# Kernel tuning notes

Measured on AMD Instinct MI355X. Metric: run time of the kernel, lower is better.

The kernel has to match this reference:

```python
import jax, jax.numpy as jnp
import numpy as np

PI = 3.141592653  # same constant as the torch source
M = 4
MIN_LAMBDA = 5.0
MAX_LAMBDA = 1500.0
IT = 1  # first forward call


def setup_inputs() -> dict:
    key = jax.random.key(0)
    k1, k2, k3 = jax.random.split(key, 3)
    N, D, C = 512, 512, 100000
    x = jax.random.normal(k1, (N, D), dtype=jnp.float32)
    target = jax.random.randint(k2, (N,), 0, C, dtype=jnp.int64)
    weight = jax.random.normal(k3, (D, C), dtype=jnp.float32)
    return {"x": x, "target": target, "weight": weight}


def reference(x, target, weight):
    # normalize weight columns (dim=0), as in F.normalize(w, p=2, dim=0)
    w = weight / jnp.linalg.norm(weight, axis=0, keepdims=True)
    w_norm = jnp.linalg.norm(w, axis=0, keepdims=True)          # [1, C] (~1)
    x_norm = jnp.linalg.norm(x, axis=1, keepdims=True)          # [N, 1]

    cos_theta = x @ w                                           # [N, C]
    cos_theta = jnp.clip(cos_theta / x_norm / w_norm, -1.0, 1.0)

    rows = jnp.arange(x.shape[0])
    c_t = cos_theta[rows, target]                               # [N]
    # m=4 multi-angle: cos(4t) = 8c^4 - 8c^2 + 1
    cos_m_theta = 8.0 * c_t ** 4 - 8.0 * c_t ** 2 + 1.0
    theta = jnp.arccos(c_t)
    k = jnp.floor(M * theta / PI)
    sign = 1.0 - 2.0 * (k % 2.0)                                # (-1)^k for integer-valued float k
    phi_t = sign * cos_m_theta - 2.0 * k

    cur_lambda = max(MIN_LAMBDA, MAX_LAMBDA / (1.0 + 0.1 * IT))
    addition = (phi_t - c_t) * x_norm[:, 0] / (1.0 + cur_lambda)

    out = cos_theta * x_norm                                    # [N, C]
    out = out.at[rows, target].add(addition)
    return out
```

## Files before the change

kernel.cpp:

```cpp
#include <hip/hip_runtime.h>
#include <hip/hip_bf16.h>

typedef __attribute__((ext_vector_type(4))) float f32x4;
typedef __attribute__((ext_vector_type(8))) short s16x8;

#define NR 512
#define KD 512
#define CC 100000
#define BN 32
#define LDSK 40

static __device__ __forceinline__ unsigned short f2bf(float f) {
    union { float f; unsigned u; } v; v.f = f;
    unsigned r = v.u + 0x7FFFu + ((v.u >> 16) & 1u);
    return (unsigned short)(r >> 16);
}

__global__ __launch_bounds__(256) void prep_kernel(const float* __restrict__ x,
                                                   float* __restrict__ xn,
                                                   unsigned short* __restrict__ xb) {
    const int row = blockIdx.x;
    const int t = threadIdx.x;
    const float* xr = x + row * KD;
    float v0 = xr[t];
    float v1 = xr[t + 256];
    float ss = v0 * v0 + v1 * v1;
    #pragma unroll
    for (int off = 32; off > 0; off >>= 1) ss += __shfl_down(ss, off, 64);
    __shared__ float sred[4];
    if ((t & 63) == 0) sred[t >> 6] = ss;
    __syncthreads();
    if (t == 0) xn[row] = sqrtf(sred[0] + sred[1] + sred[2] + sred[3]);
    xb[row * KD + t]       = f2bf(v0);
    xb[row * KD + t + 256] = f2bf(v1);
}

__global__ __launch_bounds__(256, 3) void gemm_kernel(const float* __restrict__ w,
                                                      const unsigned short* __restrict__ xb,
                                                      const float* __restrict__ xn,
                                                      float* __restrict__ out) {
    __shared__ unsigned short ldsB[BN * LDSK];
    __shared__ float sPart[8][BN];
    __shared__ float sInv[BN];

    const int t    = threadIdx.x;
    const int lane = t & 63;
    const int wv   = t >> 6;
    const int c0   = blockIdx.x * BN;
    const int cL   = t & 31;
    const int kq   = t >> 5;

    f32x4 acc[8][2];
    #pragma unroll
    for (int i = 0; i < 8; ++i) {
        acc[i][0] = {0.f, 0.f, 0.f, 0.f};
        acc[i][1] = {0.f, 0.f, 0.f, 0.f};
    }

    float ss = 0.0f;
    const int rowbase = wv * 128;
    const int arow = lane & 15;
    const int akq  = lane >> 4;

    const float* wp0 = w + (size_t)(kq * 4) * CC + c0 + cL;
    float bc0 = wp0[0];
    float bc1 = wp0[(size_t)CC];
    float bc2 = wp0[(size_t)2 * CC];
    float bc3 = wp0[(size_t)3 * CC];

    const unsigned short* abase = xb + (rowbase + arow) * KD + akq * 8;

    #pragma unroll 1
    for (int it = 0; it < 16; ++it) {
        const int kk = it * 32;

        s16x8 af[8];
        #pragma unroll
        for (int rt = 0; rt < 8; ++rt)
            af[rt] = *(const s16x8*)(abase + rt * 16 * KD + kk);

        float bn0 = 0.f, bn1 = 0.f, bn2 = 0.f, bn3 = 0.f;
        if (it < 15) {
            const float* wp = w + (size_t)(kk + 32 + kq * 4) * CC + c0 + cL;
            bn0 = wp[0];
            bn1 = wp[(size_t)CC];
            bn2 = wp[(size_t)2 * CC];
            bn3 = wp[(size_t)3 * CC];
        }

        ss += bc0 * bc0 + bc1 * bc1 + bc2 * bc2 + bc3 * bc3;
        ushort4 pk;
        pk.x = f2bf(bc0);
        pk.y = f2bf(bc1);
        pk.z = f2bf(bc2);
        pk.w = f2bf(bc3);

        __syncthreads();
        *(ushort4*)&ldsB[cL * LDSK + kq * 4] = pk;
        __syncthreads();

        const s16x8 bf0 = *(const s16x8*)&ldsB[(0 * 16 + arow) * LDSK + akq * 8];
        const s16x8 bf1 = *(const s16x8*)&ldsB[(1 * 16 + arow) * LDSK + akq * 8];

        #pragma unroll
        for (int rt = 0; rt < 8; ++rt) {
            acc[rt][0] = __builtin_amdgcn_mfma_f32_16x16x32_bf16(af[rt], bf0, acc[rt][0], 0, 0, 0);
            acc[rt][1] = __builtin_amdgcn_mfma_f32_16x16x32_bf16(af[rt], bf1, acc[rt][1], 0, 0, 0);
        }
        bc0 = bn0; bc1 = bn1; bc2 = bn2; bc3 = bn3;
    }

    sPart[kq][cL] = ss;
    __syncthreads();
    if (t < BN) {
        float tot = 0.f;
        #pragma unroll
        for (int i = 0; i < 8; ++i) tot += sPart[i][t];
        sInv[t] = 1.0f / sqrtf(tot);
    }
    __syncthreads();

    #pragma unroll
    for (int rt = 0; rt < 8; ++rt) {
        const int rbase = rowbase + rt * 16 + akq * 4;
        const f32x4 xnv = *(const f32x4*)(xn + rbase);
        #pragma unroll
        for (int ct = 0; ct < 2; ++ct) {
            const float inv = sInv[ct * 16 + arow];
            float* op = out + (size_t)rbase * CC + c0 + ct * 16 + arow;
            #pragma unroll
            for (int r = 0; r < 4; ++r) {
                float cv = acc[rt][ct][r] * inv / xnv[r];
                cv = fminf(1.0f, fmaxf(-1.0f, cv));
                op[(size_t)r * CC] = cv * xnv[r];
            }
        }
    }
}

__global__ __launch_bounds__(512) void fixup_kernel(const int* __restrict__ target,
                                                    const float* __restrict__ xn,
                                                    float* __restrict__ out) {
    const int i = threadIdx.x;
    const int tg = target[i];
    const float xni = xn[i];
    float* p = out + (size_t)i * CC + tg;
    const float val = *p;
    float c = val / xni;
    c = fminf(1.0f, fmaxf(-1.0f, c));
    const float c2 = c * c;
    const float cosm = 8.0f * c2 * c2 - 8.0f * c2 + 1.0f;
    const float theta = acosf(c);
    const float kf = floorf(4.0f * theta / 3.141592653f);
    const float sign = (((int)kf) & 1) ? -1.0f : 1.0f;
    const float phi = sign * cosm - 2.0f * kf;
    const float lam = 1500.0f / 1.1f;
    const float add = (phi - c) * xni / (1.0f + lam);
    *p = val + add;
}

extern "C" void kernel_launch(void* const* d_in, const int* in_sizes, int n_in,
                              void* d_out, int out_size, void* d_ws, size_t ws_size,
                              hipStream_t stream) {
    const float* x      = (const float*)d_in[0];
    const int*   target = (const int*)d_in[1];
    const float* w      = (const float*)d_in[2];
    float* out = (float*)d_out;

    float* xn = (float*)d_ws;
    unsigned short* xb = (unsigned short*)((char*)d_ws + 2048);

    prep_kernel<<<NR, 256, 0, stream>>>(x, xn, xb);
    gemm_kernel<<<CC / BN, 256, 0, stream>>>(w, xb, xn, out);
    fixup_kernel<<<1, 512, 0, stream>>>(target, xn, out);
}
```

Baseline: 523.4 us.

## Load weight fragments directly per wave, removing LDS staging and block barriers

Each wave now loads the full 32x32 weight tile straight from global memory into registers in MFMA B-operand layout and converts it to bf16 in registers. This removes the shared-memory staging, the two __syncthreads per K-step, and the LDS-based column-norm reduction, which is replaced by cross-lane shuffles. The cost is that each of the four waves re-reads the same weight tile, so global/L2 load traffic for weights rises fourfold and the norm-of-squares work is repeated per wave. Register pressure also grows from the 16-float prefetch buffers.

```diff
diff --git a/kernel.cpp b/kernel.cpp
--- a/kernel.cpp
+++ b/kernel.cpp
@@ -8,7 +8,6 @@
 #define KD 512
 #define CC 100000
 #define BN 32
-#define LDSK 40
 
 static __device__ __forceinline__ unsigned short f2bf(float f) {
     union { float f; unsigned u; } v; v.f = f;
@@ -39,16 +38,13 @@
                                                       const unsigned short* __restrict__ xb,
                                                       const float* __restrict__ xn,
                                                       float* __restrict__ out) {
-    __shared__ unsigned short ldsB[BN * LDSK];
-    __shared__ float sPart[8][BN];
-    __shared__ float sInv[BN];
-
     const int t    = threadIdx.x;
     const int lane = t & 63;
     const int wv   = t >> 6;
     const int c0   = blockIdx.x * BN;
-    const int cL   = t & 31;
-    const int kq   = t >> 5;
+    const int n    = lane & 15;
+    const int q    = lane >> 4;
+    const int rowbase = wv * 128;
 
     f32x4 acc[8][2];
     #pragma unroll
@@ -57,77 +53,78 @@
         acc[i][1] = {0.f, 0.f, 0.f, 0.f};
     }
 
-    float ss = 0.0f;
-    const int rowbase = wv * 128;
-    const int arow = lane & 15;
-    const int akq  = lane >> 4;
+    const unsigned short* ap[8];
+    #pragma unroll
+    for (int rt = 0; rt < 8; ++rt)
+        ap[rt] = xb + (size_t)(rowbase + rt * 16 + n) * KD + q * 8;
 
-    const float* wp0 = w + (size_t)(kq * 4) * CC + c0 + cL;
-    float bc0 = wp0[0];
-    float bc1 = wp0[(size_t)CC];
-    float bc2 = wp0[(size_t)2 * CC];
-    float bc3 = wp0[(size_t)3 * CC];
+    const float* wp = w + (size_t)(q * 8) * CC + c0 + n;
 
-    const unsigned short* abase = xb + (rowbase + arow) * KD + akq * 8;
+    float bc0[8], bc1[8];
+    #pragma unroll
+    for (int j = 0; j < 8; ++j) {
+        const float* p = wp + (size_t)j * CC;
+        bc0[j] = p[0];
+        bc1[j] = p[16];
+    }
+    wp += (size_t)32 * CC;
+
+    float ss0 = 0.f, ss1 = 0.f;
 
     #pragma unroll 1
     for (int it = 0; it < 16; ++it) {
-        const int kk = it * 32;
+        float bn0[8], bn1[8];
+        #pragma unroll
+        for (int j = 0; j < 8; ++j) { bn0[j] = 0.f; bn1[j] = 0.f; }
+        if (it < 15) {
+            #pragma unroll
+            for (int j = 0; j < 8; ++j) {
+                const float* p = wp + (size_t)j * CC;
+                bn0[j] = p[0];
+                bn1[j] = p[16];
+            }
+        }
 
         s16x8 af[8];
         #pragma unroll
         for (int rt = 0; rt < 8; ++rt)
-            af[rt] = *(const s16x8*)(abase + rt * 16 * KD + kk);
+            af[rt] = *(const s16x8*)(ap[rt] + it * 32);
 
-        float bn0 = 0.f, bn1 = 0.f, bn2 = 0.f, bn3 = 0.f;
-        if (it < 15) {
-            const float* wp = w + (size_t)(kk + 32 + kq * 4) * CC + c0 + cL;
-            bn0 = wp[0];
-            bn1 = wp[(size_t)CC];
-            bn2 = wp[(size_t)2 * CC];
-            bn3 = wp[(size_t)3 * CC];
+        s16x8 bf0, bf1;
+        #pragma unroll
+        for (int j = 0; j < 8; ++j) {
+            ss0 += bc0[j] * bc0[j];
+            ss1 += bc1[j] * bc1[j];
+            bf0[j] = (short)f2bf(bc0[j]);
+            bf1[j] = (short)f2bf(bc1[j]);
         }
-
-        ss += bc0 * bc0 + bc1 * bc1 + bc2 * bc2 + bc3 * bc3;
-        ushort4 pk;
-        pk.x = f2bf(bc0);
-        pk.y = f2bf(bc1);
-        pk.z = f2bf(bc2);
-        pk.w = f2bf(bc3);
-
-        __syncthreads();
-        *(ushort4*)&ldsB[cL * LDSK + kq * 4] = pk;
-        __syncthreads();
-
-        const s16x8 bf0 = *(const s16x8*)&ldsB[(0 * 16 + arow) * LDSK + akq * 8];
-        const s16x8 bf1 = *(const s16x8*)&ldsB[(1 * 16 + arow) * LDSK + akq * 8];
 
         #pragma unroll
         for (int rt = 0; rt < 8; ++rt) {
             acc[rt][0] = __builtin_amdgcn_mfma_f32_16x16x32_bf16(af[rt], bf0, acc[rt][0], 0, 0, 0);
             acc[rt][1] = __builtin_amdgcn_mfma_f32_16x16x32_bf16(af[rt], bf1, acc[rt][1], 0, 0, 0);
         }
-        bc0 = bn0; bc1 = bn1; bc2 = bn2; bc3 = bn3;
+
+        #pragma unroll
+        for (int j = 0; j < 8; ++j) { bc0[j] = bn0[j]; bc1[j] = bn1[j]; }
+        wp += (size_t)32 * CC;
     }
 
-    sPart[kq][cL] = ss;
-    __syncthreads();
-    if (t < BN) {
-        float tot = 0.f;
-        #pragma unroll
-        for (int i = 0; i < 8; ++i) tot += sPart[i][t];
-        sInv[t] = 1.0f / sqrtf(tot);
-    }
-    __syncthreads();
+    ss0 += __shfl_xor(ss0, 16, 64);
+    ss0 += __shfl_xor(ss0, 32, 64);
+    ss1 += __shfl_xor(ss1, 16, 64);
+    ss1 += __shfl_xor(ss1, 32, 64);
+    const float inv0 = 1.0f / sqrtf(ss0);
+    const float inv1 = 1.0f / sqrtf(ss1);
 
     #pragma unroll
     for (int rt = 0; rt < 8; ++rt) {
-        const int rbase = rowbase + rt * 16 + akq * 4;
+        const int rbase = rowbase + rt * 16 + q * 4;
         const f32x4 xnv = *(const f32x4*)(xn + rbase);
         #pragma unroll
         for (int ct = 0; ct < 2; ++ct) {
-            const float inv = sInv[ct * 16 + arow];
-            float* op = out + (size_t)rbase * CC + c0 + ct * 16 + arow;
+            const float inv = ct ? inv1 : inv0;
+            float* op = out + (size_t)rbase * CC + c0 + ct * 16 + n;
             #pragma unroll
             for (int r = 0; r < 4; ++r) {
                 float cv = acc[rt][ct][r] * inv / xnv[r];
```

New measurement: 547.1 us. 4.5% more time.
